# Kernel optimization log

Hardware: AMD Instinct MI355X
Metric: run time of the kernel (lower is better)

Reference implementation:

```python
import jax, jax.numpy as jnp
import numpy as np

TEMPERATURE = 0.5


def setup_inputs() -> dict:
    key = jax.random.key(0)
    ks = jax.random.split(key, 12)
    B, N, T = 128, 64, 256
    IN, H, OUT = N + T, 256, 128
    E = N * (N - 1) // 2  # 2016 upper-tri edges per graph
    total_edges = B * E
    inp = {
        "x_topology": jax.random.normal(ks[0], (B, N, N), jnp.float32),
        "x_temporal": jax.random.normal(ks[1], (B, N, T), jnp.float32),
        "gumbel_u": jax.random.uniform(ks[2], (total_edges,), jnp.float32, 1e-6, 1.0),
        # GNNLayer linear
        "W_gnn": jax.random.normal(ks[3], (IN, H), jnp.float32) / np.sqrt(IN),
        "b_gnn": jnp.zeros((H,), jnp.float32),
        # edge heads (input dim 2*H)
        "W_mean": jax.random.normal(ks[4], (2 * H, OUT), jnp.float32) / np.sqrt(2 * H),
        "b_mean": jnp.zeros((OUT,), jnp.float32),
        "W_var": jax.random.normal(ks[5], (2 * H, OUT), jnp.float32) / np.sqrt(2 * H),
        "b_var": jnp.zeros((OUT,), jnp.float32),
        "W_w": jax.random.normal(ks[6], (2 * H, 1), jnp.float32) / np.sqrt(2 * H),
        "b_w": jnp.zeros((1,), jnp.float32),
    }
    return inp


def reference(x_topology, x_temporal, gumbel_u, W_gnn, b_gnn,
              W_mean, b_mean, W_var, b_var, W_w, b_w):
    B, N, _ = x_topology.shape
    T = x_temporal.shape[-1]
    # Upper-triangular fully-connected edge index (no self loops), batched with node offsets.
    row, col = jnp.triu_indices(N, k=1)          # [E]
    E = row.shape[0]
    offs = (jnp.arange(B) * N)[:, None]          # [B,1]
    src = (row[None, :] + offs).reshape(-1)       # [B*E]
    dst = (col[None, :] + offs).reshape(-1)       # [B*E]

    # Node features: concat topology + temporal, flatten batch of graphs.
    x = jnp.concatenate([x_topology, x_temporal], axis=-1).reshape(B * N, N + T)

    # Mean aggregation (PyG aggr='mean'): messages x[src] scattered to dst; 0 for isolated nodes.
    msg_sum = jax.ops.segment_sum(x[src], dst, num_segments=B * N)      # [B*N, N+T]
    cnt = jax.ops.segment_sum(jnp.ones_like(src, x.dtype), dst, num_segments=B * N)
    agg = jnp.where(cnt[:, None] > 0, msg_sum / jnp.maximum(cnt, 1.0)[:, None], 0.0)

    h = jax.nn.relu(agg @ W_gnn + b_gnn)          # [B*N, H]

    # Edge MLP heads on gathered [src||dst] embeddings.
    ef = jnp.concatenate([h[src], h[dst]], axis=-1)        # [B*E, 2H]
    mean = ef @ W_mean + b_mean                             # [B*E, OUT]
    variance = jax.nn.softplus(ef @ W_var + b_var) + 1e-6   # [B*E, OUT]
    weight = jax.nn.sigmoid((ef @ W_w + b_w)[:, 0])          # [B*E]

    # Gumbel-softmax over the flattened edge-weight vector (dim=-1 of a 1-D tensor).
    g = -jnp.log(-jnp.log(gumbel_u))
    gumbel_w = jax.nn.softmax((weight + g) / TEMPERATURE, axis=-1)

    # Gaussian similarity per edge, scatter into dense adjacency.
    sim = jnp.exp(-0.5 * jnp.mean(mean ** 2 / (variance + 1e-8), axis=-1))
    edge_w = sim * gumbel_w                                  # [B*E]

    b_idx = jnp.repeat(jnp.arange(B), E)
    adj = jnp.zeros((B, N, N), x.dtype).at[b_idx, jnp.tile(row, B), jnp.tile(col, B)].set(edge_w)
    return adj
```

## Files before the change

kernel.cpp:

```cpp
#include <hip/hip_runtime.h>
#include <hip/hip_bf16.h>
#include <math.h>

#define Bg   128
#define Nn   64
#define Tt   256
#define INF  320
#define Hd   256
#define OUTD 128
#define Ee   2016
#define TOTE (Bg*Ee)
#define SCOLS 576
#define MROWS 8192

#define RSQRT_LN2 1.2011224087864498f
#define LOG2E     1.4426950408889634f
#define EPS_T     1.45719e-6f

typedef __attribute__((ext_vector_type(8))) short bf16x8;
typedef __attribute__((ext_vector_type(4))) float f32x4;

static __device__ __forceinline__ ushort f2bf(float v) {
    __hip_bfloat16 h = __float2bfloat16(v);
    return *(ushort*)&h;
}

#define CVT_N (INF * Hd)
#define PACK_N (Hd * SCOLS)
__global__ void k_prep(const float* __restrict__ Wg, const float* __restrict__ Wm,
                       const float* __restrict__ Wv, const float* __restrict__ Ww,
                       const float* __restrict__ bm, const float* __restrict__ bv,
                       const float* __restrict__ bw,
                       ushort* __restrict__ WgbT, ushort* __restrict__ WcatT,
                       float* __restrict__ ebias, unsigned* __restrict__ red) {
    int idx = blockIdx.x * 256 + threadIdx.x;
    if (idx == 0) { red[0] = 0u; red[1] = 0u; }
    if (idx < CVT_N) {
        int n = idx / INF, k = idx - n * INF;
        WgbT[idx] = f2bf(Wg[k * Hd + n]);
        return;
    }
    idx -= CVT_N;
    if (idx < PACK_N) {
        int n = idx / Hd, k = idx - n * Hd;
        float v = 0.f;
        if (n < 128)       v = Wm[k * 128 + n];
        else if (n < 256)  v = Wm[(256 + k) * 128 + (n - 128)];
        else if (n < 384)  v = Wv[k * 128 + (n - 256)];
        else if (n < 512)  v = Wv[(256 + k) * 128 + (n - 384)];
        else if (n == 512) v = Ww[k];
        else if (n == 513) v = Ww[256 + k];
        WcatT[idx] = f2bf(v);
        return;
    }
    idx -= PACK_N;
    if (idx >= SCOLS) return;
    float e = 0.f;
    if (idx < 128)                    e = bm[idx];
    else if (idx >= 256 && idx < 384) e = bv[idx - 256];
    else if (idx == 512)              e = bw[0];
    ebias[idx] = e;
}

__global__ __launch_bounds__(256) void k_agg(const float* __restrict__ topo,
                                             const float* __restrict__ temp,
                                             ushort* __restrict__ agg) {
    __shared__ float T[64 * 65];
    const int b = blockIdx.x, ft = blockIdx.y;
    const int tid = threadIdx.x;
    const int row = tid >> 2, seg = tid & 3;
    const float* src = (ft == 0) ? (topo + (size_t)(b * Nn + row) * Nn)
                                 : (temp + (size_t)(b * Nn + row) * Tt + (ft - 1) * 64);
    #pragma unroll
    for (int i = 0; i < 4; ++i) {
        float4 v = *(const float4*)(src + seg * 16 + i * 4);
        float* d = &T[row * 65 + seg * 16 + i * 4];
        d[0] = v.x; d[1] = v.y; d[2] = v.z; d[3] = v.w;
    }
    __syncthreads();
    const int w = tid >> 6, lane = tid & 63;
    #pragma unroll
    for (int k = 0; k < 16; ++k) {
        int f = w * 16 + k;
        float x = T[lane * 65 + f];
        float incl = x;
        #pragma unroll
        for (int o = 1; o < 64; o <<= 1) {
            float t = __shfl_up(incl, o);
            if (lane >= o) incl += t;
        }
        float excl = incl - x;
        T[lane * 65 + f] = lane ? excl * __builtin_amdgcn_rcpf((float)lane) : 0.f;
    }
    __syncthreads();
    const int node = tid >> 2, f0 = (tid & 3) * 16;
    ushort tmp[16];
    #pragma unroll
    for (int i = 0; i < 16; ++i) tmp[i] = f2bf(T[node * 65 + f0 + i]);
    ushort* dst = agg + (size_t)(b * Nn + node) * INF + ft * 64 + f0;
    *(uint4*)dst = *(uint4*)tmp;
    *(uint4*)(dst + 8) = *(uint4*)(tmp + 8);
}

__global__ __launch_bounds__(256) void k_gemm_mfma(const ushort* __restrict__ A,
                                                   const ushort* __restrict__ BT,
                                                   const float* __restrict__ bias,
                                                   ushort* __restrict__ Cb,
                                                   float* __restrict__ Cf,
                                                   int N, int K, int relu, int transC,
                                                   int edgeScale) {
    __shared__ ushort Asl[64 * 72];
    __shared__ ushort Bsl[64 * 72];
    const int tid = threadIdx.x;
    const int w = tid >> 6, lane = tid & 63;
    const int quad = lane >> 4, r16 = lane & 15;
    const int m0 = blockIdx.y * 64, n0 = blockIdx.x * 64;
    const int row = tid >> 2, seg = tid & 3;
    f32x4 acc[4] = {};

    for (int k0 = 0; k0 < K; k0 += 64) {
        const ushort* ap = A + (size_t)(m0 + row) * K + k0 + seg * 16;
        uint4 a0 = ((const uint4*)ap)[0];
        uint4 a1 = ((const uint4*)ap)[1];
        *(uint4*)(Asl + row * 72 + seg * 16)     = a0;
        *(uint4*)(Asl + row * 72 + seg * 16 + 8) = a1;
        const ushort* bp = BT + (size_t)(n0 + row) * K + k0 + seg * 16;
        uint4 b0 = ((const uint4*)bp)[0];
        uint4 b1 = ((const uint4*)bp)[1];
        *(uint4*)(Bsl + row * 72 + seg * 16)     = b0;
        *(uint4*)(Bsl + row * 72 + seg * 16 + 8) = b1;
        __syncthreads();

        bf16x8 af0 = *(const bf16x8*)(Asl + (w * 16 + r16) * 72 + quad * 8);
        bf16x8 af1 = *(const bf16x8*)(Asl + (w * 16 + r16) * 72 + 32 + quad * 8);
        #pragma unroll
        for (int ns = 0; ns < 4; ++ns) {
            bf16x8 bf0 = *(const bf16x8*)(Bsl + (ns * 16 + r16) * 72 + quad * 8);
            bf16x8 bf1 = *(const bf16x8*)(Bsl + (ns * 16 + r16) * 72 + 32 + quad * 8);
            acc[ns] = __builtin_amdgcn_mfma_f32_16x16x32_bf16(af0, bf0, acc[ns], 0, 0, 0);
            acc[ns] = __builtin_amdgcn_mfma_f32_16x16x32_bf16(af1, bf1, acc[ns], 0, 0, 0);
        }
        __syncthreads();
    }

    const int row0 = m0 + w * 16 + quad * 4;
    #pragma unroll
    for (int ns = 0; ns < 4; ++ns) {
        f32x4 a = acc[ns];
        int col = n0 + ns * 16 + r16;
        float bb = bias ? bias[col] : 0.f;
        float vv[4];
        #pragma unroll
        for (int i = 0; i < 4; ++i) {
            float v = a[i] + bb;
            if (relu) v = fmaxf(v, 0.f);
            vv[i] = v;
        }
        if (transC) {
            if (edgeScale) {
                if (col < 256) {
                    #pragma unroll
                    for (int i = 0; i < 4; ++i) vv[i] *= RSQRT_LN2;
                } else if (col < 512) {
                    #pragma unroll
                    for (int i = 0; i < 4; ++i)
                        vv[i] = __builtin_amdgcn_exp2f(vv[i] * LOG2E);
                }
            }
            *(float4*)(Cf + (size_t)col * MROWS + row0) = make_float4(vv[0], vv[1], vv[2], vv[3]);
        } else {
            #pragma unroll
            for (int i = 0; i < 4; ++i) {
                int row2 = row0 + i;
                if (Cb) Cb[(size_t)row2 * N + col] = f2bf(vv[i]);
                else    Cf[(size_t)row2 * N + col] = vv[i];
            }
        }
    }
}

static __device__ __forceinline__ float et(float mA, float mB, float eA, float eB) {
    float m = mA + mB;
    float E = eA * eB;
    float t = __builtin_amdgcn_logf(1.f + E) + EPS_T;
    return m * m * __builtin_amdgcn_rcpf(t);
}

__global__ __launch_bounds__(512, 2) void k_edge5(const float* __restrict__ ST,
                                                  float* __restrict__ accp) {
    __shared__ float L[4][64][36];
    const int bid = blockIdx.x;
    const int b = bid >> 2, oc = bid & 3;
    const int tid = threadIdx.x;

    {
        const int c = (tid >> 4) & 31, q = tid & 15, n = q << 2;
        const int s0 = c ^ ((((n    ) >> 1) & 7) << 2);
        const int s1 = c ^ ((((n + 1) >> 1) & 7) << 2);
        const int s2 = c ^ ((((n + 2) >> 1) & 7) << 2);
        const int s3 = c ^ ((((n + 3) >> 1) & 7) << 2);
        #pragma unroll
        for (int arr = 0; arr < 4; ++arr) {
            float4 v = *(const float4*)&ST[(size_t)(arr * 128 + oc * 32 + c) * MROWS
                                           + b * 64 + n];
            L[arr][n + 0][s0] = v.x;
            L[arr][n + 1][s1] = v.y;
            L[arr][n + 2][s2] = v.z;
            L[arr][n + 3][s3] = v.w;
        }
    }

    const bool strict = tid < 496;
    int ri0, ri1, rj0, rj1;
    if (strict) {
        int rr = tid, ci = 0;
        while (rr >= 31 - ci) { rr -= 31 - ci; ++ci; }
        int cj = ci + 1 + rr;
        ri0 = 2 * ci; ri1 = ri0 + 1;
        rj0 = 2 * cj; rj1 = rj0 + 1;
    } else {
        int d0 = (tid - 496) * 2, d1 = d0 + 1;
        ri0 = 2 * d0; rj0 = ri0 + 1;
        ri1 = 2 * d1; rj1 = ri1 + 1;
    }
    const float* M0 = &L[0][ri0][0]; const float* M1 = &L[0][ri1][0];
    const float* N0 = &L[1][rj0][0]; const float* N1 = &L[1][rj1][0];
    const float* E0 = &L[2][ri0][0]; const float* E1 = &L[2][ri1][0];
    const float* F0 = &L[3][rj0][0]; const float* F1 = &L[3][rj1][0];
    const int si0 = ((ri0 >> 1) & 7) << 2, si1 = ((ri1 >> 1) & 7) << 2;
    const int sj0 = ((rj0 >> 1) & 7) << 2, sj1 = ((rj1 >> 1) & 7) << 2;

    __syncthreads();

    float a00 = 0.f, a01 = 0.f, a10 = 0.f, a11 = 0.f;
    #pragma unroll 2
    for (int t = 0; t < 32; t += 4) {
        float4 m0 = *(const float4*)(M0 + (t ^ si0));
        float4 m1 = *(const float4*)(M1 + (t ^ si1));
        float4 n0 = *(const float4*)(N0 + (t ^ sj0));
        float4 n1 = *(const float4*)(N1 + (t ^ sj1));
        float4 e0 = *(const float4*)(E0 + (t ^ si0));
        float4 e1 = *(const float4*)(E1 + (t ^ si1));
        float4 f0 = *(const float4*)(F0 + (t ^ sj0));
        float4 f1 = *(const float4*)(F1 + (t ^ sj1));
        a00 += et(m0.x,n0.x,e0.x,f0.x) + et(m0.y,n0.y,e0.y,f0.y)
             + et(m0.z,n0.z,e0.z,f0.z) + et(m0.w,n0.w,e0.w,f0.w);
        a11 += et(m1.x,n1.x,e1.x,f1.x) + et(m1.y,n1.y,e1.y,f1.y)
             + et(m1.z,n1.z,e1.z,f1.z) + et(m1.w,n1.w,e1.w,f1.w);
        if (strict) {
            a01 += et(m0.x,n1.x,e0.x,f1.x) + et(m0.y,n1.y,e0.y,f1.y)
                 + et(m0.z,n1.z,e0.z,f1.z) + et(m0.w,n1.w,e0.w,f1.w);
            a10 += et(m1.x,n0.x,e1.x,f0.x) + et(m1.y,n0.y,e1.y,f0.y)
                 + et(m1.z,n0.z,e1.z,f0.z) + et(m1.w,n0.w,e1.w,f0.w);
        }
    }

    float* ap = accp + (size_t)oc * TOTE + (size_t)b * Ee;
    if (strict) {
        int e0i = (ri0 * (127 - ri0)) / 2 + (rj0 - ri0 - 1);
        int e1i = (ri1 * (127 - ri1)) / 2 + (rj0 - ri1 - 1);
        ap[e0i] = a00; ap[e0i + 1] = a01;
        ap[e1i] = a10; ap[e1i + 1] = a11;
    } else {
        ap[(ri0 * (127 - ri0)) / 2] = a00;
        ap[(ri1 * (127 - ri1)) / 2] = a11;
    }
}

__global__ __launch_bounds__(256) void k_den(const float* __restrict__ ST,
                                             const float* __restrict__ gu,
                                             float* __restrict__ numer,
                                             unsigned* __restrict__ red) {
    __shared__ float sred[4];
    const int tid = threadIdx.x;
    int idx = blockIdx.x * 256 + tid;
    int b = idx >> 12, rem = idx & 4095;
    int r = rem >> 6, c = rem & 63;
    float en = 0.f;
    if (c > r) {
        int e = b * Ee + (r * (127 - r)) / 2 + (c - r - 1);
        float wr = ST[(size_t)512 * MROWS + b * 64 + r]
                 + ST[(size_t)513 * MROWS + b * 64 + c];
        float w  = __builtin_amdgcn_rcpf(1.f + __expf(-wr));
        float g  = -__logf(-__logf(gu[e]));
        en = __expf((w + g) * 2.0f);
        numer[e] = en;
    }
    float s = en;
    #pragma unroll
    for (int o = 32; o; o >>= 1) s += __shfl_down(s, o);
    if ((tid & 63) == 0) sred[tid >> 6] = s;
    __syncthreads();
    if (tid == 0) atomicAdd((float*)&red[1], sred[0] + sred[1] + sred[2] + sred[3]);
}

__global__ void k_out(const float* __restrict__ accp, const float* __restrict__ numer,
                      const unsigned* __restrict__ red, float* __restrict__ out) {
    int idx = blockIdx.x * 256 + threadIdx.x;
    if (idx >= Bg * Nn * Nn) return;
    int b = idx >> 12;
    int rem = idx & 4095;
    int r = rem >> 6, c = rem & 63;
    float v = 0.f;
    if (c > r) {
        int e = b * Ee + (r * (127 - r)) / 2 + (c - r - 1);
        float a = accp[e] + accp[TOTE + e] + accp[2 * TOTE + e] + accp[3 * TOTE + e];
        float se = __expf(a * (-1.f / 256.f));
        float Sinv = __builtin_amdgcn_rcpf(((const float*)red)[1]);
        v = se * numer[e] * Sinv;
    }
    out[idx] = v;
}

extern "C" void kernel_launch(void* const* d_in, const int* in_sizes, int n_in,
                              void* d_out, int out_size, void* d_ws, size_t ws_size,
                              hipStream_t stream) {
    const float* topo = (const float*)d_in[0];
    const float* temp = (const float*)d_in[1];
    const float* gu   = (const float*)d_in[2];
    const float* Wg   = (const float*)d_in[3];
    const float* bg   = (const float*)d_in[4];
    const float* Wm   = (const float*)d_in[5];
    const float* bm   = (const float*)d_in[6];
    const float* Wv   = (const float*)d_in[7];
    const float* bv   = (const float*)d_in[8];
    const float* Ww   = (const float*)d_in[9];
    const float* bw   = (const float*)d_in[10];
    float* out = (float*)d_out;

    char* ws = (char*)d_ws;
    size_t off = 0;
    auto carve = [&](size_t bytes) { char* p = ws + off; off = (off + bytes + 255) & ~(size_t)255; return p; };

    char*   r1    = carve((size_t)SCOLS * MROWS * 4);
    float*  ST    = (float*)r1;
    ushort* aggb  = (ushort*)r1;
    ushort* hb    = (ushort*)carve((size_t)MROWS * Hd * 2);
    ushort* WgbT  = (ushort*)carve((size_t)INF * Hd * 2);
    ushort* WcatT = (ushort*)carve((size_t)Hd * SCOLS * 2);
    float*  ebias = (float*)carve((size_t)SCOLS * 4);
    float*  numer = (float*)carve((size_t)TOTE * 4);
    float*  accp  = (float*)carve((size_t)4 * TOTE * 4);
    unsigned* red = (unsigned*)carve(256);

    k_prep<<<(CVT_N + PACK_N + SCOLS + 255) / 256, 256, 0, stream>>>(
        Wg, Wm, Wv, Ww, bm, bv, bw, WgbT, WcatT, ebias, red);
    k_agg<<<dim3(Bg, INF / 64), 256, 0, stream>>>(topo, temp, aggb);
    k_gemm_mfma<<<dim3(Hd / 64, MROWS / 64), 256, 0, stream>>>(
        aggb, WgbT, bg, hb, nullptr, Hd, INF, 1, 0, 0);
    k_gemm_mfma<<<dim3(SCOLS / 64, MROWS / 64), 256, 0, stream>>>(
        hb, WcatT, ebias, nullptr, ST, SCOLS, Hd, 0, 1, 1);
    k_edge5<<<Bg * 4, 512, 0, stream>>>(ST, accp);
    k_den<<<(Bg * Nn * Nn) / 256, 256, 0, stream>>>(ST, gu, numer, red);
    k_out<<<(Bg * Nn * Nn + 255) / 256, 256, 0, stream>>>(accp, numer, red, out);
}
```

Baseline: 157.4 us.

## Split edge kernel into 32x32 node-pair tiles with XCD-aware block mapping

The pairwise edge kernel now runs one 256-thread block per (graph, 32x32 tile, output chunk) instead of one 512-thread block per (graph, output chunk). That is three tiles per graph: two diagonal triangles and one full off-diagonal square. Shared memory per block is halved and the grid grows to 1536 blocks, which should improve occupancy and load balance. Block ids are remapped so that blocks from the same graph land on the same XCD, for L2 locality. In the triangle tiles many threads sit idle, and some staging work is repeated across tiles.

Measured after the change: 155.6 us. Within noise of the previous version (-1.1%).

```diff
diff --git a/kernel.cpp b/kernel.cpp
--- a/kernel.cpp
+++ b/kernel.cpp
@@ -186,84 +186,94 @@
     return m * m * __builtin_amdgcn_rcpf(t);
 }
 
-__global__ __launch_bounds__(512, 2) void k_edge5(const float* __restrict__ ST,
+static __device__ __forceinline__ float et4(float4 ma, float4 mb, float4 ea, float4 eb) {
+    return et(ma.x, mb.x, ea.x, eb.x) + et(ma.y, mb.y, ea.y, eb.y)
+         + et(ma.z, mb.z, ea.z, eb.z) + et(ma.w, mb.w, ea.w, eb.w);
+}
+
+__global__ __launch_bounds__(256, 4) void k_edge6(const float* __restrict__ ST,
                                                   float* __restrict__ accp) {
-    __shared__ float L[4][64][36];
+    __shared__ float L[4][32][36];
     const int bid = blockIdx.x;
-    const int b = bid >> 2, oc = bid & 3;
+    const int xcd = bid & 7, kk = bid >> 3;
+    const int b = xcd * 16 + kk / 12;
+    const int sub = kk - (kk / 12) * 12;
+    const int tile = sub >> 2, oc = sub & 3;
+    const int g0 = (tile == 2) ? 1 : 0;
+    const int g1 = (tile == 0) ? 0 : 1;
     const int tid = threadIdx.x;
 
     {
-        const int c = (tid >> 4) & 31, q = tid & 15, n = q << 2;
-        const int s0 = c ^ ((((n    ) >> 1) & 7) << 2);
-        const int s1 = c ^ ((((n + 1) >> 1) & 7) << 2);
-        const int s2 = c ^ ((((n + 2) >> 1) & 7) << 2);
-        const int s3 = c ^ ((((n + 3) >> 1) & 7) << 2);
+        const int c = tid >> 3, n4 = (tid & 7) << 2;
         #pragma unroll
         for (int arr = 0; arr < 4; ++arr) {
+            const int g = (arr & 1) ? g1 : g0;
             float4 v = *(const float4*)&ST[(size_t)(arr * 128 + oc * 32 + c) * MROWS
-                                           + b * 64 + n];
-            L[arr][n + 0][s0] = v.x;
-            L[arr][n + 1][s1] = v.y;
-            L[arr][n + 2][s2] = v.z;
-            L[arr][n + 3][s3] = v.w;
-        }
-    }
-
-    const bool strict = tid < 496;
-    int ri0, ri1, rj0, rj1;
-    if (strict) {
-        int rr = tid, ci = 0;
-        while (rr >= 31 - ci) { rr -= 31 - ci; ++ci; }
-        int cj = ci + 1 + rr;
-        ri0 = 2 * ci; ri1 = ri0 + 1;
-        rj0 = 2 * cj; rj1 = rj0 + 1;
+                                           + b * 64 + g * 32 + n4];
+            #pragma unroll
+            for (int di = 0; di < 4; ++di) {
+                const int n = n4 + di;
+                const int sw = ((n >> 1) & 7) << 2;
+                L[arr][n][c ^ sw] = ((const float*)&v)[di];
+            }
+        }
+    }
+
+    bool valid, diagcell = false;
+    int i0, j0;
+    if (g0 != g1) {
+        valid = true;
+        i0 = (tid >> 4) * 2; j0 = (tid & 15) * 2;
+    } else if (tid < 120) {
+        valid = true;
+        int ii = 0, rr = tid;
+        while (rr >= 15 - ii) { rr -= 15 - ii; ++ii; }
+        i0 = ii * 2; j0 = (ii + 1 + rr) * 2;
+    } else if (tid < 136) {
+        valid = true; diagcell = true;
+        int d = tid - 120;
+        i0 = 2 * d; j0 = 2 * d + 1;
     } else {
-        int d0 = (tid - 496) * 2, d1 = d0 + 1;
-        ri0 = 2 * d0; rj0 = ri0 + 1;
-        ri1 = 2 * d1; rj1 = ri1 + 1;
-    }
-    const float* M0 = &L[0][ri0][0]; const float* M1 = &L[0][ri1][0];
-    const float* N0 = &L[1][rj0][0]; const float* N1 = &L[1][rj1][0];
-    const float* E0 = &L[2][ri0][0]; const float* E1 = &L[2][ri1][0];
-    const float* F0 = &L[3][rj0][0]; const float* F1 = &L[3][rj1][0];
-    const int si0 = ((ri0 >> 1) & 7) << 2, si1 = ((ri1 >> 1) & 7) << 2;
-    const int sj0 = ((rj0 >> 1) & 7) << 2, sj1 = ((rj1 >> 1) & 7) << 2;
+        valid = false; i0 = 0; j0 = 2;
+    }
+    const int i1 = diagcell ? i0 : i0 + 1;
+    const int j1 = diagcell ? j0 : j0 + 1;
+    const int swi0 = ((i0 >> 1) & 7) << 2, swi1 = ((i1 >> 1) & 7) << 2;
+    const int swj0 = ((j0 >> 1) & 7) << 2, swj1 = ((j1 >> 1) & 7) << 2;
 
     __syncthreads();
 
     float a00 = 0.f, a01 = 0.f, a10 = 0.f, a11 = 0.f;
-    #pragma unroll 2
-    for (int t = 0; t < 32; t += 4) {
-        float4 m0 = *(const float4*)(M0 + (t ^ si0));
-        float4 m1 = *(const float4*)(M1 + (t ^ si1));
-        float4 n0 = *(const float4*)(N0 + (t ^ sj0));
-        float4 n1 = *(const float4*)(N1 + (t ^ sj1));
-        float4 e0 = *(const float4*)(E0 + (t ^ si0));
-        float4 e1 = *(const float4*)(E1 + (t ^ si1));
-        float4 f0 = *(const float4*)(F0 + (t ^ sj0));
-        float4 f1 = *(const float4*)(F1 + (t ^ sj1));
-        a00 += et(m0.x,n0.x,e0.x,f0.x) + et(m0.y,n0.y,e0.y,f0.y)
-             + et(m0.z,n0.z,e0.z,f0.z) + et(m0.w,n0.w,e0.w,f0.w);
-        a11 += et(m1.x,n1.x,e1.x,f1.x) + et(m1.y,n1.y,e1.y,f1.y)
-             + et(m1.z,n1.z,e1.z,f1.z) + et(m1.w,n1.w,e1.w,f1.w);
-        if (strict) {
-            a01 += et(m0.x,n1.x,e0.x,f1.x) + et(m0.y,n1.y,e0.y,f1.y)
-                 + et(m0.z,n1.z,e0.z,f1.z) + et(m0.w,n1.w,e0.w,f1.w);
-            a10 += et(m1.x,n0.x,e1.x,f0.x) + et(m1.y,n0.y,e1.y,f0.y)
-                 + et(m1.z,n0.z,e1.z,f0.z) + et(m1.w,n0.w,e1.w,f0.w);
-        }
-    }
-
-    float* ap = accp + (size_t)oc * TOTE + (size_t)b * Ee;
-    if (strict) {
-        int e0i = (ri0 * (127 - ri0)) / 2 + (rj0 - ri0 - 1);
-        int e1i = (ri1 * (127 - ri1)) / 2 + (rj0 - ri1 - 1);
-        ap[e0i] = a00; ap[e0i + 1] = a01;
-        ap[e1i] = a10; ap[e1i + 1] = a11;
-    } else {
-        ap[(ri0 * (127 - ri0)) / 2] = a00;
-        ap[(ri1 * (127 - ri1)) / 2] = a11;
+    if (valid) {
+        #pragma unroll 2
+        for (int t = 0; t < 32; t += 4) {
+            float4 mi0 = *(const float4*)&L[0][i0][t ^ swi0];
+            float4 mi1 = *(const float4*)&L[0][i1][t ^ swi1];
+            float4 mj0 = *(const float4*)&L[1][j0][t ^ swj0];
+            float4 mj1 = *(const float4*)&L[1][j1][t ^ swj1];
+            float4 ei0 = *(const float4*)&L[2][i0][t ^ swi0];
+            float4 ei1 = *(const float4*)&L[2][i1][t ^ swi1];
+            float4 ej0 = *(const float4*)&L[3][j0][t ^ swj0];
+            float4 ej1 = *(const float4*)&L[3][j1][t ^ swj1];
+            a00 += et4(mi0, mj0, ei0, ej0);
+            a01 += et4(mi0, mj1, ei0, ej1);
+            a10 += et4(mi1, mj0, ei1, ej0);
+            a11 += et4(mi1, mj1, ei1, ej1);
+        }
+    }
+
+    if (valid) {
+        const int ni0 = g0 * 32 + i0, ni1 = g0 * 32 + i1;
+        const int nj0 = g1 * 32 + j0;
+        float* ap = accp + (size_t)oc * TOTE + (size_t)b * Ee;
+        if (diagcell) {
+            ap[(ni0 * (127 - ni0)) / 2 + (nj0 - ni0 - 1)] = a00;
+        } else {
+            int e0 = (ni0 * (127 - ni0)) / 2 + (nj0 - ni0 - 1);
+            int e1 = (ni1 * (127 - ni1)) / 2 + (nj0 - ni1 - 1);
+            ap[e0] = a00; ap[e0 + 1] = a01;
+            ap[e1] = a10; ap[e1 + 1] = a11;
+        }
     }
 }
 
@@ -350,7 +360,7 @@
         aggb, WgbT, bg, hb, nullptr, Hd, INF, 1, 0, 0);
     k_gemm_mfma<<<dim3(SCOLS / 64, MROWS / 64), 256, 0, stream>>>(
         hb, WcatT, ebias, nullptr, ST, SCOLS, Hd, 0, 1, 1);
-    k_edge5<<<Bg * 4, 512, 0, stream>>>(ST, accp);
+    k_edge6<<<Bg * 12, 256, 0, stream>>>(ST, accp);
     k_den<<<(Bg * Nn * Nn) / 256, 256, 0, stream>>>(ST, gu, numer, red);
     k_out<<<(Bg * Nn * Nn + 255) / 256, 256, 0, stream>>>(accp, numer, red, out);
 }
```
